# Kernel optimization log

Hardware: AMD Instinct MI355X
Metric: run time of the kernel (lower is better)

The kernel has to match this reference:

```python
import jax, jax.numpy as jnp
import numpy as np

NUM_USERS = 30000
NUM_ITEMS = 30000
N = NUM_USERS + NUM_ITEMS          # total graph nodes (users + items)
E = 800000                          # number of edges
EMBED_K = 64
INTENTS = 4
D = EMBED_K // INTENTS              # per-intent channel chunk
N_LAYERS = 1
ROUTING_ITERS = 2


def setup_inputs() -> dict:
    key = jax.random.key(0)
    k1, k2, k3, k4 = jax.random.split(key, 4)
    Gu = jax.random.normal(k1, (NUM_USERS, EMBED_K), jnp.float32) * 0.1
    Gi = jax.random.normal(k2, (NUM_ITEMS, EMBED_K), jnp.float32) * 0.1
    # head list: guarantee every node appears at least once as a head so that
    # D = 1/sqrt(row_degree) is finite (real CF graphs have no isolated rows)
    edge_h = jnp.concatenate([jnp.arange(N, dtype=jnp.int64),
                              jax.random.randint(k3, (E - N,), 0, N, dtype=jnp.int64)])
    edge_t = jax.random.randint(k4, (E,), 0, N, dtype=jnp.int64)
    return {"Gu": Gu, "Gi": Gi, "edge_h": edge_h, "edge_t": edge_t}


def _l2norm(x, eps=1e-12):
    # matches torch.nn.functional.normalize(dim=-1)
    return x / jnp.sqrt(jnp.maximum(jnp.sum(x * x, axis=-1, keepdims=True), eps))


def reference(Gu, Gi, edge_h, edge_t):
    ego = jnp.concatenate([Gu, Gi], axis=0)            # [N, K]
    all_emb = [ego]
    # routing attention logits per intent per edge (initialized to ones)
    A_values = jnp.ones((INTENTS, E), dtype=Gu.dtype)
    for _ in range(N_LAYERS):
        # split embed dim into INTENTS contiguous chunks -> [I, N, D]
        X = ego.reshape(N, INTENTS, D).transpose(1, 0, 2)
        Z = X
        for _t in range(ROUTING_ITERS):
            # softmax over intents per edge (pick=False path; p_train is always False)
            scores = jax.nn.softmax(A_values, axis=0)                    # [I, E]
            # per-intent row degrees (sparse.sum over dim=1 indexes rows = heads)
            deg = jnp.zeros((INTENTS, N), scores.dtype).at[:, edge_h].add(scores)
            d_col = 1.0 / jnp.sqrt(deg)                                  # [I, N]
            # D_col @ X, A @ (.), D_col @ (.)  -- note original applies D_col twice (as written)
            Y = d_col[..., None] * X                                     # [I, N, D]
            msg = scores[..., None] * Y[:, edge_t, :]                    # [I, E, D]
            Z = jnp.zeros((INTENTS, N, D), X.dtype).at[:, edge_h, :].add(msg)
            Z = d_col[..., None] * Z                                     # [I, N, D]
            # attention update: normalize(head) . tanh(normalize(tail))
            head = _l2norm(Z[:, edge_h, :])                              # [I, E, D]
            tail = _l2norm(X[:, edge_t, :])                              # [I, E, D]
            A_values = A_values + jnp.sum(head * jnp.tanh(tail), axis=-1)
        # concat intent chunks back along channel dim
        ego = Z.transpose(1, 0, 2).reshape(N, EMBED_K)
        all_emb.append(ego)
    out = jnp.mean(jnp.stack(all_emb, axis=1), axis=1)   # [N, K]
    return out[:NUM_USERS], out[NUM_USERS:]
```

## Files before the change

kernel.cpp:

```cpp
#include <hip/hip_runtime.h>
#include <hip/hip_fp16.h>


#define NUSERS 30000
#define NN     60000
#define EE     800000
#define SL     ((size_t)NN * 16)
#define SLY    ((size_t)(NN + 1) * 32)
#define SCAN_B ((NN + 255) / 256)
#define EV_B   ((EE / 4 + 255) / 256)
#define NW1_B  ((NN + 1 + 3) / 4)
#define OUTG   ((NN + 31) / 32)
#define OUT_B  ((((OUTG + 1) / 2) * 8))

__device__ __forceinline__ float getX(const float* __restrict__ Gu,
                                      const float* __restrict__ Gi,
                                      int n, int c) {
    return (n < NUSERS) ? Gu[n * 64 + c] : Gi[(n - NUSERS) * 64 + c];
}

__device__ __forceinline__ int clampN(int n) {
    return ((unsigned)n < (unsigned)NN) ? n : 0;
}

__device__ __forceinline__ __half2 shfl_xor_h2(__half2 x, int m) {
    int xi = __builtin_bit_cast(int, x);
    xi = __shfl_xor(xi, m, 64);
    return __builtin_bit_cast(__half2, xi);
}

__device__ __forceinline__ int pinnedNode(int b, int tid, int* i) {
    int xcd = b & 7;
    *i = xcd >> 1;
    int g = (b >> 3) * 2 + (xcd & 1);
    return g * 4 + (tid >> 6);
}


__global__ void edge_count(const int* __restrict__ eh, int* __restrict__ deg0) {
    int e4 = (blockIdx.x * blockDim.x + threadIdx.x) * 4;
    if (e4 >= EE) return;
    int4 h = *(const int4*)(eh + e4);
    atomicAdd(&deg0[clampN(h.x)], 1);
    atomicAdd(&deg0[clampN(h.y)], 1);
    atomicAdd(&deg0[clampN(h.z)], 1);
    atomicAdd(&deg0[clampN(h.w)], 1);
}

__global__ void scan_local(const int* __restrict__ deg0, int* __restrict__ offsets,
                           int* __restrict__ bsum, int* __restrict__ cursor) {
    int gid = blockIdx.x * 256 + threadIdx.x;
    int lane = threadIdx.x & 63, w = threadIdx.x >> 6;
    int vdeg = (gid < NN) ? deg0[gid] : 0;
    if (gid < NN) cursor[gid] = 0;
    int x = vdeg;
    #pragma unroll
    for (int d = 1; d < 64; d <<= 1) {
        int y = __shfl_up(x, d, 64);
        if (lane >= d) x += y;
    }
    __shared__ int wsum[4];
    if (lane == 63) wsum[w] = x;
    __syncthreads();
    int wpre = 0;
    #pragma unroll
    for (int j = 0; j < 4; ++j) wpre += (j < w) ? wsum[j] : 0;
    int incl = x + wpre;
    if (gid < NN) offsets[gid] = incl - vdeg;
    if (threadIdx.x == 255) bsum[blockIdx.x] = incl;
}

__global__ void scan_add2(int* __restrict__ offsets, const int* __restrict__ bsum) {
    int tid = threadIdx.x, lane = tid & 63, w = tid >> 6;
    int vv = (tid < SCAN_B) ? bsum[tid] : 0;
    int x = vv;
    #pragma unroll
    for (int d = 1; d < 64; d <<= 1) {
        int y = __shfl_up(x, d, 64);
        if (lane >= d) x += y;
    }
    __shared__ int wsum[4];
    __shared__ int bpre;
    if (lane == 63) wsum[w] = x;
    __syncthreads();
    int wpre = 0;
    #pragma unroll
    for (int j = 0; j < 4; ++j) wpre += (j < w) ? wsum[j] : 0;
    if (tid == blockIdx.x) bpre = x + wpre - vv;
    __syncthreads();
    int gid = blockIdx.x * 256 + tid;
    if (gid < NN) offsets[gid] += bpre;
    if (gid == 0) offsets[NN] = EE;
}

__global__ void scatter_prep(const int* __restrict__ eh, const int* __restrict__ et,
                             const int* __restrict__ offsets, int* __restrict__ cursor,
                             int* __restrict__ csr_tail,
                             const float* __restrict__ Gu, const float* __restrict__ Gi,
                             const int* __restrict__ deg0, __half* __restrict__ YT) {
    if (blockIdx.x < EV_B) {
        int e4 = (blockIdx.x * 256 + threadIdx.x) * 4;
        if (e4 >= EE) return;
        int4 h = *(const int4*)(eh + e4);
        int4 t = *(const int4*)(et + e4);
        int h0 = clampN(h.x), h1 = clampN(h.y), h2 = clampN(h.z), h3 = clampN(h.w);
        int s0 = offsets[h0] + atomicAdd(&cursor[h0], 1);
        if (s0 < EE) csr_tail[s0] = clampN(t.x);
        int s1 = offsets[h1] + atomicAdd(&cursor[h1], 1);
        if (s1 < EE) csr_tail[s1] = clampN(t.y);
        int s2 = offsets[h2] + atomicAdd(&cursor[h2], 1);
        if (s2 < EE) csr_tail[s2] = clampN(t.z);
        int s3 = offsets[h3] + atomicAdd(&cursor[h3], 1);
        if (s3 < EE) csr_tail[s3] = clampN(t.w);
    } else {
        int n = (blockIdx.x - EV_B) * 4 + (threadIdx.x >> 6);
        if (n > NN) return;
        int lane = threadIdx.x & 63;
        int i = lane >> 4, ch = lane & 15;
        float x = (n < NN) ? getX(Gu, Gi, n, lane) : 0.f;
        float sx = x * x;
        #pragma unroll
        for (int m = 1; m < 16; m <<= 1) sx += __shfl_xor(sx, m, 64);
        float invx = rsqrtf(fmaxf(sx, 1e-12f));
        float d0 = rsqrtf(fmaxf(0.25f * (float)((n < NN) ? deg0[n] : 1), 1e-30f));
        size_t a = (size_t)i * SLY + (size_t)n * 32 + (size_t)(ch >> 2) * 8 + (ch & 3);
        YT[a]     = __float2half(d0 * x);
        YT[a + 4] = __float2half(tanhf(x * invx));
    }
}

__global__ void fused_attn(const int* __restrict__ offsets, const int* __restrict__ csr_tail,
                           const __half* __restrict__ YT, __half* __restrict__ v) {
    int i;
    int n = pinnedNode(blockIdx.x, threadIdx.x, &i);
    int lane = threadIdx.x & 63;
    int e4 = lane >> 2, cp = lane & 3;
    int s0 = offsets[n], s1 = offsets[n + 1];
    int deg = s1 - s0;
    const __half* Yi = YT + (size_t)i * SLY;
    const __half2 h2z = __floats2half2_rn(0.f, 0.f);

    __half2 z0 = h2z, z1 = h2z;
    __half2 tA0 = h2z, tA1 = h2z, tB0 = h2z, tB1 = h2z;
    bool actA = false, actB = false;
    bool fast = (deg <= 32);

    if (fast) {
        int kkA = s0 + e4; actA = kkA < s1;
        int tA = actA ? csr_tail[kkA] : NN;
        const __half2* rA = (const __half2*)(Yi + (size_t)tA * 32 + cp * 8);
        z0 = rA[0]; z1 = rA[1]; tA0 = rA[2]; tA1 = rA[3];
        if (deg > 16) {
            int kkB = s0 + 16 + e4; actB = kkB < s1;
            int tB = actB ? csr_tail[kkB] : NN;
            const __half2* rB = (const __half2*)(Yi + (size_t)tB * 32 + cp * 8);
            z0 = __hadd2(z0, rB[0]); z1 = __hadd2(z1, rB[1]);
            tB0 = rB[2]; tB1 = rB[3];
        }
    } else {
        for (int base = s0; base < s1; base += 16) {
            int kk = base + e4;
            int t = (kk < s1) ? csr_tail[kk] : NN;
            const __half2* r = (const __half2*)(Yi + (size_t)t * 32 + cp * 8);
            z0 = __hadd2(z0, r[0]); z1 = __hadd2(z1, r[1]);
        }
    }
    #pragma unroll
    for (int m = 4; m < 64; m <<= 1) {
        z0 = __hadd2(z0, shfl_xor_h2(z0, m));
        z1 = __hadd2(z1, shfl_xor_h2(z1, m));
    }
    float2 f0 = __half22float2(z0), f1 = __half22float2(z1);
    float ss = f0.x * f0.x + f0.y * f0.y + f1.x * f1.x + f1.y * f1.y;
    ss += __shfl_xor(ss, 1, 64);
    ss += __shfl_xor(ss, 2, 64);
    float inv = rsqrtf(fmaxf(ss, 1e-12f));
    __half2 zn0 = __floats2half2_rn(f0.x * inv, f0.y * inv);
    __half2 zn1 = __floats2half2_rn(f1.x * inv, f1.y * inv);

    __half* vi = v + (size_t)i * EE;
    if (fast) {
        __half2 d2 = __hmul2(zn0, tA0); d2 = __hfma2(zn1, tA1, d2);
        float2 df = __half22float2(d2);
        float p = df.x + df.y;
        p += __shfl_xor(p, 1, 64);
        p += __shfl_xor(p, 2, 64);
        if (actA && cp == 0) vi[s0 + e4] = __float2half(p);
        if (deg > 16) {
            __half2 e2 = __hmul2(zn0, tB0); e2 = __hfma2(zn1, tB1, e2);
            float2 ef = __half22float2(e2);
            float q = ef.x + ef.y;
            q += __shfl_xor(q, 1, 64);
            q += __shfl_xor(q, 2, 64);
            if (actB && cp == 0) vi[s0 + 16 + e4] = __float2half(q);
        }
    } else {
        for (int base = s0; base < s1; base += 16) {
            int kk = base + e4;
            bool act = kk < s1;
            int t = act ? csr_tail[kk] : NN;
            const __half2* r = (const __half2*)(Yi + (size_t)t * 32 + cp * 8 + 4);
            __half2 d2 = __hmul2(zn0, r[0]); d2 = __hfma2(zn1, r[1], d2);
            float2 df = __half22float2(d2);
            float p = df.x + df.y;
            p += __shfl_xor(p, 1, 64);
            p += __shfl_xor(p, 2, 64);
            if (act && cp == 0) vi[kk] = __float2half(p);
        }
    }
}

__global__ void sm_dcol_y1(const int* __restrict__ offsets, const __half* __restrict__ v,
                           __half* __restrict__ scores, float* __restrict__ dcol1,
                           const float* __restrict__ Gu, const float* __restrict__ Gi,
                           __half* __restrict__ Y1s) {
    int n = blockIdx.x * 4 + (threadIdx.x >> 6);
    if (n >= NN) return;
    int lane = threadIdx.x & 63;
    int s0 = offsets[n], s1 = offsets[n + 1];
    float sum0 = 0.f, sum1 = 0.f, sum2 = 0.f, sum3 = 0.f;
    for (int k = s0 + lane; k < s1; k += 64) {
        float v0 = __half2float(v[k]);
        float v1 = __half2float(v[EE + k]);
        float v2 = __half2float(v[2 * EE + k]);
        float v3 = __half2float(v[3 * EE + k]);
        float mx = fmaxf(fmaxf(v0, v1), fmaxf(v2, v3));
        float e0 = __expf(v0 - mx), e1 = __expf(v1 - mx);
        float e2 = __expf(v2 - mx), e3 = __expf(v3 - mx);
        float inv = 1.f / (e0 + e1 + e2 + e3);
        e0 *= inv; e1 *= inv; e2 *= inv; e3 *= inv;
        scores[k]          = __float2half(e0);
        scores[EE + k]     = __float2half(e1);
        scores[2 * EE + k] = __float2half(e2);
        scores[3 * EE + k] = __float2half(e3);
        sum0 += e0; sum1 += e1; sum2 += e2; sum3 += e3;
    }
    #pragma unroll
    for (int m = 1; m < 64; m <<= 1) {
        sum0 += __shfl_xor(sum0, m, 64);
        sum1 += __shfl_xor(sum1, m, 64);
        sum2 += __shfl_xor(sum2, m, 64);
        sum3 += __shfl_xor(sum3, m, 64);
    }
    int i = lane >> 4, ch = lane & 15;
    float dsel = (i == 0) ? sum0 : (i == 1) ? sum1 : (i == 2) ? sum2 : sum3;
    float d = rsqrtf(fmaxf(dsel, 1e-30f));
    if (lane < 4) {
        float ds = (lane == 0) ? sum0 : (lane == 1) ? sum1 : (lane == 2) ? sum2 : sum3;
        dcol1[n * 4 + lane] = rsqrtf(fmaxf(ds, 1e-30f));
    }
    float x = getX(Gu, Gi, n, lane);
    Y1s[(size_t)i * SL + (size_t)n * 16 + ch] = __float2half(d * x);
}

__global__ void outk(const int* __restrict__ offsets, const int* __restrict__ csr_tail,
                     const __half* __restrict__ Y1s, const __half* __restrict__ scores,
                     const float* __restrict__ dcol1,
                     const float* __restrict__ Gu, const float* __restrict__ Gi,
                     float* __restrict__ out) {
    int b = blockIdx.x, tid = threadIdx.x;
    int xcd = b & 7;
    int i = xcd >> 1;
    int g = (b >> 3) * 2 + (xcd & 1);
    if (g >= OUTG) return;
    int lane = tid & 63;
    int c = lane & 7;
    int n = g * 32 + (tid >> 6) * 8 + (lane >> 3);
    if (n >= NN) return;
    int s0 = offsets[n], s1 = offsets[n + 1];
    int deg = s1 - s0;
    int md = deg;
    md = max(md, __shfl_xor(md, 8, 64));
    md = max(md, __shfl_xor(md, 16, 64));
    md = max(md, __shfl_xor(md, 32, 64));
    const __half* Yi = Y1s + (size_t)i * SL;
    const __half* si = scores + (size_t)i * EE;
    float accx = 0.f, accy = 0.f;
    for (int j = 0; j < md; j += 8) {
        int base = s0 + j;
        #pragma unroll
        for (int u = 0; u < 8; ++u) {
            int kk = base + u;
            bool act = kk < s1;
            int kc = act ? kk : s0;
            int t = csr_tail[kc];
            float s = act ? __half2float(si[kc]) : 0.f;
            __half2 y = *(const __half2*)(Yi + (size_t)t * 16 + c * 2);
            float2 yf = __half22float2(y);
            accx = fmaf(s, yf.x, accx);
            accy = fmaf(s, yf.y, accy);
        }
    }
    float d = dcol1[n * 4 + i];
    int ch = i * 16 + c * 2;
    const float* xr = (n < NUSERS) ? (Gu + n * 64 + ch) : (Gi + (n - NUSERS) * 64 + ch);
    float2 x2 = *(const float2*)xr;
    float2 o;
    o.x = 0.5f * (x2.x + d * accx);
    o.y = 0.5f * (x2.y + d * accy);
    *(float2*)(out + (size_t)n * 64 + ch) = o;
}


extern "C" void kernel_launch(void* const* d_in, const int* in_sizes, int n_in,
                              void* d_out, int out_size, void* d_ws, size_t ws_size,
                              hipStream_t stream) {
    const float* Gu = (const float*)d_in[0];
    const float* Gi = (const float*)d_in[1];
    const int* eh = (const int*)d_in[2];
    const int* et = (const int*)d_in[3];
    float* out = (float*)d_out;

    char* p = (char*)d_ws;
    __half* v        = (__half*)p;     p += (size_t)EE * 4 * 2;
    __half* scores   = (__half*)p;     p += (size_t)EE * 4 * 2;
    int*    csr_tail = (int*)p;        p += (size_t)EE * 4;
    int*    offsets  = (int*)p;        p += ((size_t)(NN + 1) * 4 + 15) / 16 * 16;
    int*    deg0     = (int*)p;        p += (size_t)NN * 4;
    int*    cursor   = (int*)p;        p += (size_t)NN * 4;
    int*    bsum     = (int*)p;        p += ((size_t)SCAN_B * 4 + 15) / 16 * 16;
    float*  dcol1    = (float*)p;      p += (size_t)NN * 4 * 4;
    __half* YT       = (__half*)p;
    __half* Y1s      = YT;

    const int nw_blocks = (NN + 3) / 4;
    const int sl_blocks = NN;

    hipMemsetAsync(deg0, 0, NN * sizeof(int), stream);
    edge_count<<<EV_B, 256, 0, stream>>>(eh, deg0);
    scan_local<<<SCAN_B, 256, 0, stream>>>(deg0, offsets, bsum, cursor);
    scan_add2<<<SCAN_B, 256, 0, stream>>>(offsets, bsum);

    scatter_prep<<<EV_B + NW1_B, 256, 0, stream>>>(eh, et, offsets, cursor, csr_tail,
                                                   Gu, Gi, deg0, YT);

    fused_attn<<<sl_blocks, 256, 0, stream>>>(offsets, csr_tail, YT, v);

    sm_dcol_y1<<<nw_blocks, 256, 0, stream>>>(offsets, v, scores, dcol1, Gu, Gi, Y1s);

    outk<<<OUT_B, 256, 0, stream>>>(offsets, csr_tail, Y1s, scores, dcol1, Gu, Gi, out);
}
```

Before: 284.9 us.

## Split fused attention into node aggregation and edge-parallel dot kernels

Replaces the per-intent, per-node fused attention kernel with two kernels. The first sums neighbor Y rows per node across all 64 channels and writes a normalized Z table. The second is edge-parallel: it reads head Z and tail tanh rows, computes all four intent dots, and writes them interleaved as 4 halfs per edge. Tables become node-major with 64 contiguous channels, which lets softmax read one 8-byte vector per edge. The cost is an extra csr_head array, an extra ZN round-trip through memory, and a second pass of random gathers over edges.

```diff
diff --git a/kernel.cpp b/kernel.cpp
--- a/kernel.cpp
+++ b/kernel.cpp
@@ -6,7 +6,6 @@
 #define NN     60000
 #define EE     800000
 #define SL     ((size_t)NN * 16)
-#define SLY    ((size_t)(NN + 1) * 32)
 #define SCAN_B ((NN + 255) / 256)
 #define EV_B   ((EE / 4 + 255) / 256)
 #define NW1_B  ((NN + 1 + 3) / 4)
@@ -23,17 +22,8 @@
     return ((unsigned)n < (unsigned)NN) ? n : 0;
 }
 
-__device__ __forceinline__ __half2 shfl_xor_h2(__half2 x, int m) {
-    int xi = __builtin_bit_cast(int, x);
-    xi = __shfl_xor(xi, m, 64);
-    return __builtin_bit_cast(__half2, xi);
-}
-
-__device__ __forceinline__ int pinnedNode(int b, int tid, int* i) {
-    int xcd = b & 7;
-    *i = xcd >> 1;
-    int g = (b >> 3) * 2 + (xcd & 1);
-    return g * 4 + (tid >> 6);
+__device__ __forceinline__ __half2 bch2(float f) {
+    return __builtin_bit_cast(__half2, f);
 }
 
 
@@ -95,9 +85,10 @@
 
 __global__ void scatter_prep(const int* __restrict__ eh, const int* __restrict__ et,
                              const int* __restrict__ offsets, int* __restrict__ cursor,
-                             int* __restrict__ csr_tail,
+                             int* __restrict__ csr_tail, int* __restrict__ csr_head,
                              const float* __restrict__ Gu, const float* __restrict__ Gi,
-                             const int* __restrict__ deg0, __half* __restrict__ YT) {
+                             const int* __restrict__ deg0,
+                             __half* __restrict__ Ytab, __half* __restrict__ Ttab) {
     if (blockIdx.x < EV_B) {
         int e4 = (blockIdx.x * 256 + threadIdx.x) * 4;
         if (e4 >= EE) return;
@@ -105,112 +96,93 @@
         int4 t = *(const int4*)(et + e4);
         int h0 = clampN(h.x), h1 = clampN(h.y), h2 = clampN(h.z), h3 = clampN(h.w);
         int s0 = offsets[h0] + atomicAdd(&cursor[h0], 1);
-        if (s0 < EE) csr_tail[s0] = clampN(t.x);
+        if (s0 < EE) { csr_tail[s0] = clampN(t.x); csr_head[s0] = h0; }
         int s1 = offsets[h1] + atomicAdd(&cursor[h1], 1);
-        if (s1 < EE) csr_tail[s1] = clampN(t.y);
+        if (s1 < EE) { csr_tail[s1] = clampN(t.y); csr_head[s1] = h1; }
         int s2 = offsets[h2] + atomicAdd(&cursor[h2], 1);
-        if (s2 < EE) csr_tail[s2] = clampN(t.z);
+        if (s2 < EE) { csr_tail[s2] = clampN(t.z); csr_head[s2] = h2; }
         int s3 = offsets[h3] + atomicAdd(&cursor[h3], 1);
-        if (s3 < EE) csr_tail[s3] = clampN(t.w);
+        if (s3 < EE) { csr_tail[s3] = clampN(t.w); csr_head[s3] = h3; }
     } else {
         int n = (blockIdx.x - EV_B) * 4 + (threadIdx.x >> 6);
         if (n > NN) return;
         int lane = threadIdx.x & 63;
-        int i = lane >> 4, ch = lane & 15;
         float x = (n < NN) ? getX(Gu, Gi, n, lane) : 0.f;
         float sx = x * x;
         #pragma unroll
         for (int m = 1; m < 16; m <<= 1) sx += __shfl_xor(sx, m, 64);
         float invx = rsqrtf(fmaxf(sx, 1e-12f));
         float d0 = rsqrtf(fmaxf(0.25f * (float)((n < NN) ? deg0[n] : 1), 1e-30f));
-        size_t a = (size_t)i * SLY + (size_t)n * 32 + (size_t)(ch >> 2) * 8 + (ch & 3);
-        YT[a]     = __float2half(d0 * x);
-        YT[a + 4] = __float2half(tanhf(x * invx));
-    }
-}
-
-__global__ void fused_attn(const int* __restrict__ offsets, const int* __restrict__ csr_tail,
-                           const __half* __restrict__ YT, __half* __restrict__ v) {
-    int i;
-    int n = pinnedNode(blockIdx.x, threadIdx.x, &i);
+        size_t a = (size_t)n * 64 + lane;
+        Ytab[a] = __float2half(d0 * x);
+        Ttab[a] = __float2half(tanhf(x * invx));
+    }
+}
+
+__global__ void zacc(const int* __restrict__ offsets, const int* __restrict__ csr_tail,
+                     const __half* __restrict__ Ytab, __half* __restrict__ ZN) {
+    int n = blockIdx.x * 4 + (threadIdx.x >> 6);
+    if (n >= NN) return;
     int lane = threadIdx.x & 63;
-    int e4 = lane >> 2, cp = lane & 3;
+    int e2 = lane >> 5, cc = lane & 31;
     int s0 = offsets[n], s1 = offsets[n + 1];
-    int deg = s1 - s0;
-    const __half* Yi = YT + (size_t)i * SLY;
-    const __half2 h2z = __floats2half2_rn(0.f, 0.f);
-
-    __half2 z0 = h2z, z1 = h2z;
-    __half2 tA0 = h2z, tA1 = h2z, tB0 = h2z, tB1 = h2z;
-    bool actA = false, actB = false;
-    bool fast = (deg <= 32);
-
-    if (fast) {
-        int kkA = s0 + e4; actA = kkA < s1;
-        int tA = actA ? csr_tail[kkA] : NN;
-        const __half2* rA = (const __half2*)(Yi + (size_t)tA * 32 + cp * 8);
-        z0 = rA[0]; z1 = rA[1]; tA0 = rA[2]; tA1 = rA[3];
-        if (deg > 16) {
-            int kkB = s0 + 16 + e4; actB = kkB < s1;
-            int tB = actB ? csr_tail[kkB] : NN;
-            const __half2* rB = (const __half2*)(Yi + (size_t)tB * 32 + cp * 8);
-            z0 = __hadd2(z0, rB[0]); z1 = __hadd2(z1, rB[1]);
-            tB0 = rB[2]; tB1 = rB[3];
-        }
-    } else {
-        for (int base = s0; base < s1; base += 16) {
-            int kk = base + e4;
-            int t = (kk < s1) ? csr_tail[kk] : NN;
-            const __half2* r = (const __half2*)(Yi + (size_t)t * 32 + cp * 8);
-            z0 = __hadd2(z0, r[0]); z1 = __hadd2(z1, r[1]);
-        }
-    }
-    #pragma unroll
-    for (int m = 4; m < 64; m <<= 1) {
-        z0 = __hadd2(z0, shfl_xor_h2(z0, m));
-        z1 = __hadd2(z1, shfl_xor_h2(z1, m));
-    }
-    float2 f0 = __half22float2(z0), f1 = __half22float2(z1);
-    float ss = f0.x * f0.x + f0.y * f0.y + f1.x * f1.x + f1.y * f1.y;
+    float accx = 0.f, accy = 0.f;
+    for (int base = s0; base < s1; base += 2) {
+        int kk = base + e2;
+        bool act = kk < s1;
+        int kc = (kk < EE) ? kk : (EE - 1);
+        int t = act ? csr_tail[kc] : NN;
+        __half2 y = *(const __half2*)(Ytab + (size_t)t * 64 + cc * 2);
+        float2 yf = __half22float2(y);
+        accx += yf.x; accy += yf.y;
+    }
+    accx += __shfl_xor(accx, 32, 64);
+    accy += __shfl_xor(accy, 32, 64);
+    float ss = accx * accx + accy * accy;
     ss += __shfl_xor(ss, 1, 64);
     ss += __shfl_xor(ss, 2, 64);
+    ss += __shfl_xor(ss, 4, 64);
     float inv = rsqrtf(fmaxf(ss, 1e-12f));
-    __half2 zn0 = __floats2half2_rn(f0.x * inv, f0.y * inv);
-    __half2 zn1 = __floats2half2_rn(f1.x * inv, f1.y * inv);
-
-    __half* vi = v + (size_t)i * EE;
-    if (fast) {
-        __half2 d2 = __hmul2(zn0, tA0); d2 = __hfma2(zn1, tA1, d2);
-        float2 df = __half22float2(d2);
-        float p = df.x + df.y;
-        p += __shfl_xor(p, 1, 64);
-        p += __shfl_xor(p, 2, 64);
-        if (actA && cp == 0) vi[s0 + e4] = __float2half(p);
-        if (deg > 16) {
-            __half2 e2 = __hmul2(zn0, tB0); e2 = __hfma2(zn1, tB1, e2);
-            float2 ef = __half22float2(e2);
-            float q = ef.x + ef.y;
-            q += __shfl_xor(q, 1, 64);
-            q += __shfl_xor(q, 2, 64);
-            if (actB && cp == 0) vi[s0 + 16 + e4] = __float2half(q);
-        }
-    } else {
-        for (int base = s0; base < s1; base += 16) {
-            int kk = base + e4;
-            bool act = kk < s1;
-            int t = act ? csr_tail[kk] : NN;
-            const __half2* r = (const __half2*)(Yi + (size_t)t * 32 + cp * 8 + 4);
-            __half2 d2 = __hmul2(zn0, r[0]); d2 = __hfma2(zn1, r[1], d2);
-            float2 df = __half22float2(d2);
-            float p = df.x + df.y;
-            p += __shfl_xor(p, 1, 64);
-            p += __shfl_xor(p, 2, 64);
-            if (act && cp == 0) vi[kk] = __float2half(p);
-        }
-    }
-}
-
-__global__ void sm_dcol_y1(const int* __restrict__ offsets, const __half* __restrict__ v,
+    if (lane < 32) {
+        *(__half2*)(ZN + (size_t)n * 64 + cc * 2) =
+            __floats2half2_rn(accx * inv, accy * inv);
+    }
+}
+
+__global__ void attdot(const int* __restrict__ csr_head, const int* __restrict__ csr_tail,
+                       const __half* __restrict__ ZN, const __half* __restrict__ Ttab,
+                       __half* __restrict__ v4) {
+    int k = blockIdx.x * 256 + threadIdx.x;
+    if (k >= EE) return;
+    int h = csr_head[k], t = csr_tail[k];
+    const float4* zp = (const float4*)(ZN + (size_t)h * 64);
+    const float4* tp = (const float4*)(Ttab + (size_t)t * 64);
+    float dot[4];
+    #pragma unroll
+    for (int i = 0; i < 4; ++i) {
+        float4 za = zp[2 * i], zb = zp[2 * i + 1];
+        float4 ta = tp[2 * i], tb = tp[2 * i + 1];
+        __half2 acc = __floats2half2_rn(0.f, 0.f);
+        acc = __hfma2(bch2(za.x), bch2(ta.x), acc);
+        acc = __hfma2(bch2(za.y), bch2(ta.y), acc);
+        acc = __hfma2(bch2(za.z), bch2(ta.z), acc);
+        acc = __hfma2(bch2(za.w), bch2(ta.w), acc);
+        acc = __hfma2(bch2(zb.x), bch2(tb.x), acc);
+        acc = __hfma2(bch2(zb.y), bch2(tb.y), acc);
+        acc = __hfma2(bch2(zb.z), bch2(tb.z), acc);
+        acc = __hfma2(bch2(zb.w), bch2(tb.w), acc);
+        float2 f = __half22float2(acc);
+        dot[i] = f.x + f.y;
+    }
+    __half2 o01 = __floats2half2_rn(dot[0], dot[1]);
+    __half2 o23 = __floats2half2_rn(dot[2], dot[3]);
+    int2 st;
+    st.x = __builtin_bit_cast(int, o01);
+    st.y = __builtin_bit_cast(int, o23);
+    *(int2*)(v4 + (size_t)k * 4) = st;
+}
+
+__global__ void sm_dcol_y1(const int* __restrict__ offsets, const __half* __restrict__ v4,
                            __half* __restrict__ scores, float* __restrict__ dcol1,
                            const float* __restrict__ Gu, const float* __restrict__ Gi,
                            __half* __restrict__ Y1s) {
@@ -220,10 +192,11 @@
     int s0 = offsets[n], s1 = offsets[n + 1];
     float sum0 = 0.f, sum1 = 0.f, sum2 = 0.f, sum3 = 0.f;
     for (int k = s0 + lane; k < s1; k += 64) {
-        float v0 = __half2float(v[k]);
-        float v1 = __half2float(v[EE + k]);
-        float v2 = __half2float(v[2 * EE + k]);
-        float v3 = __half2float(v[3 * EE + k]);
+        int2 raw = *(const int2*)(v4 + (size_t)k * 4);
+        __half2 p01 = __builtin_bit_cast(__half2, raw.x);
+        __half2 p23 = __builtin_bit_cast(__half2, raw.y);
+        float2 fa = __half22float2(p01), fb = __half22float2(p23);
+        float v0 = fa.x, v1 = fa.y, v2 = fb.x, v3 = fb.y;
         float mx = fmaxf(fmaxf(v0, v1), fmaxf(v2, v3));
         float e0 = __expf(v0 - mx), e1 = __expf(v1 - mx);
         float e2 = __expf(v2 - mx), e3 = __expf(v3 - mx);
@@ -312,19 +285,21 @@
     float* out = (float*)d_out;
 
     char* p = (char*)d_ws;
-    __half* v        = (__half*)p;     p += (size_t)EE * 4 * 2;
+    __half* v4       = (__half*)p;     p += (size_t)EE * 4 * 2;
     __half* scores   = (__half*)p;     p += (size_t)EE * 4 * 2;
     int*    csr_tail = (int*)p;        p += (size_t)EE * 4;
+    int*    csr_head = (int*)p;        p += (size_t)EE * 4;
     int*    offsets  = (int*)p;        p += ((size_t)(NN + 1) * 4 + 15) / 16 * 16;
     int*    deg0     = (int*)p;        p += (size_t)NN * 4;
     int*    cursor   = (int*)p;        p += (size_t)NN * 4;
     int*    bsum     = (int*)p;        p += ((size_t)SCAN_B * 4 + 15) / 16 * 16;
     float*  dcol1    = (float*)p;      p += (size_t)NN * 4 * 4;
-    __half* YT       = (__half*)p;
-    __half* Y1s      = YT;
+    __half* Ytab     = (__half*)p;     p += (size_t)(NN + 1) * 64 * 2;
+    __half* Ttab     = (__half*)p;     p += (size_t)(NN + 1) * 64 * 2;
+    __half* ZN       = (__half*)p;
+    __half* Y1s      = Ytab;
 
     const int nw_blocks = (NN + 3) / 4;
-    const int sl_blocks = NN;
 
     hipMemsetAsync(deg0, 0, NN * sizeof(int), stream);
     edge_count<<<EV_B, 256, 0, stream>>>(eh, deg0);
@@ -332,11 +307,12 @@
     scan_add2<<<SCAN_B, 256, 0, stream>>>(offsets, bsum);
 
     scatter_prep<<<EV_B + NW1_B, 256, 0, stream>>>(eh, et, offsets, cursor, csr_tail,
-                                                   Gu, Gi, deg0, YT);
-
-    fused_attn<<<sl_blocks, 256, 0, stream>>>(offsets, csr_tail, YT, v);
-
-    sm_dcol_y1<<<nw_blocks, 256, 0, stream>>>(offsets, v, scores, dcol1, Gu, Gi, Y1s);
+                                                   csr_head, Gu, Gi, deg0, Ytab, Ttab);
+
+    zacc<<<nw_blocks, 256, 0, stream>>>(offsets, csr_tail, Ytab, ZN);
+    attdot<<<(EE + 255) / 256, 256, 0, stream>>>(csr_head, csr_tail, ZN, Ttab, v4);
+
+    sm_dcol_y1<<<nw_blocks, 256, 0, stream>>>(offsets, v4, scores, dcol1, Gu, Gi, Y1s);
 
     outk<<<OUT_B, 256, 0, stream>>>(offsets, csr_tail, Y1s, scores, dcol1, Gu, Gi, out);
 }
```

Result: slower. 295.4 us (+3.7%).
